# Optimization experiments

Hardware: AMD Instinct MI355X
Metric: run time of the kernel (lower is better)

Reference implementation:

```python
import jax, jax.numpy as jnp
import numpy as np

EMBED_DIM = 64
NUM_HEADS = 8
D_K = EMBED_DIM // NUM_HEADS  # 8
B, S = 8, 1024


def setup_inputs() -> dict:
    key = jax.random.key(0)
    ks = jax.random.split(key, 10)
    f32 = jnp.float32
    lim = 1.0 / np.sqrt(EMBED_DIM)
    def lin(k):
        kw, kb = jax.random.split(k)
        w = jax.random.uniform(kw, (EMBED_DIM, EMBED_DIM), f32, -lim, lim)
        b = jax.random.uniform(kb, (EMBED_DIM,), f32, -lim, lim)
        return w, b
    wq, bq = lin(ks[0])
    wk, bk = lin(ks[1])
    wv, bv = lin(ks[2])
    wo, bo = lin(ks[3])
    theta = jax.random.normal(ks[4], (EMBED_DIM,), f32)  # trainable RY angles, one per wire
    x = jax.random.normal(ks[5], (B, S, EMBED_DIM), f32)
    return {"x": x, "wq": wq, "bq": bq, "wk": wk, "bk": bk,
            "wv": wv, "bv": bv, "theta": theta, "wo": wo, "bo": bo}


def _quantum_map(t, theta):
    # Per-qubit circuit on |0>: RX(t_i) encode, RY(theta_i), <PauliZ_i>.
    # Product state => <Z_i> = cos(theta_i) * cos(t_i) exactly.
    return jnp.cos(theta) * jnp.cos(t.reshape(-1, EMBED_DIM))  # [N, E]


def reference(x, wq, bq, wk, bk, wv, bv, theta, wo, bo):
    # Linear QKV (torch nn.Linear: x @ W^T + b)
    q = x @ wq.T + bq
    k = x @ wk.T + bk
    v = x @ wv.T + bv
    # Quantum measurement map, flattened over batch*seq (as in the original)
    q_q = _quantum_map(q, theta)  # [N, E], N = B*S
    k_q = _quantum_map(k, theta)
    v_q = _quantum_map(v, theta)
    # Full flattened attention: [N, N] scores (original never reshapes back)
    scores = (q_q @ k_q.T) / jnp.sqrt(jnp.asarray(D_K, x.dtype))
    attn = jax.nn.softmax(scores, axis=-1)  # dropout is identity in eval
    out = attn @ v_q  # [N, E]
    return out @ wo.T + bo
```

## Files before the change

kernel.cpp:

```cpp
#include <hip/hip_runtime.h>
#include <hip/hip_bf16.h>

#define NQ 8192
#define DIM 64
#define SPLITS 16
#define QBLK 128
#define WQ 64
#define BN 64
#define KEYS_PER_SPLIT (NQ / SPLITS)
#define NTILES (KEYS_PER_SPLIT / BN)
#define GRID_FLASH ((NQ / QBLK) * SPLITS)
#define MERGEB 256
#define MROWS (NQ / MERGEB)
#define SC2 0.51012301920911057f
#define KSTR 72

typedef short s8v __attribute__((ext_vector_type(8)));
typedef short s4v __attribute__((ext_vector_type(4)));
typedef float f4v __attribute__((ext_vector_type(4)));
typedef int   i4v __attribute__((ext_vector_type(4)));
typedef int   i2v __attribute__((ext_vector_type(2)));

__device__ __forceinline__ float b2f(short s) {
  unsigned int u = ((unsigned int)(unsigned short)s) << 16;
  return __uint_as_float(u);
}
__device__ __forceinline__ short f2b(float f) {
  __hip_bfloat16 h = __float2bfloat16(f);
  return *reinterpret_cast<short*>(&h);
}
__device__ __forceinline__ int pack_bf16x2(float a, float b) {
  union { __hip_bfloat162 h; int i; } u;
  u.h = __float22bfloat162_rn(make_float2(a, b));
  return u.i;
}

#define QROWS 16
__global__ __launch_bounds__(256) void qkv_kernel(
    const float* __restrict__ x,
    const float* __restrict__ wq, const float* __restrict__ bq,
    const float* __restrict__ wk, const float* __restrict__ bk,
    const float* __restrict__ wv, const float* __restrict__ bv,
    const float* __restrict__ theta,
    short* __restrict__ qq, short* __restrict__ kvT) {
  __shared__ __align__(16) short wsh[3][DIM][KSTR];
  __shared__ __align__(16) short xsb[QROWS][DIM];
  int tid = threadIdx.x;
  for (int i = tid; i < 3 * DIM * 16; i += 256) {
    int m = i >> 10;
    int rem = i & 1023;
    int r = rem >> 4, c4 = (rem & 15) << 2;
    const float* src = (m == 0) ? wq : (m == 1) ? wk : wv;
    float4 w = *(const float4*)&src[r * DIM + c4];
    s4v p = {f2b(w.x), f2b(w.y), f2b(w.z), f2b(w.w)};
    *(s4v*)&wsh[m][r][c4] = p;
  }
  int rowbase = blockIdx.x * QROWS;
  for (int i = tid; i < QROWS * 16; i += 256) {
    int r = i >> 4, c4 = (i & 15) << 2;
    float4 v = *(const float4*)&x[(rowbase + r) * DIM + c4];
    s4v p = {f2b(v.x), f2b(v.y), f2b(v.z), f2b(v.w)};
    *(s4v*)&xsb[r][c4] = p;
  }
  __syncthreads();
  int e = tid & 63, rg = tid >> 6;
  float ct = __cosf(theta[e]);
  float bqv = bq[e], bkv = bk[e], bvv = bv[e];
  for (int r = rg; r < QROWS; r += 4) {
    float aq = bqv, ak = bkv, av = bvv;
#pragma unroll
    for (int c8 = 0; c8 < 8; ++c8) {
      s8v xv = *(const s8v*)&xsb[r][c8 * 8];
      s8v w0 = *(const s8v*)&wsh[0][e][c8 * 8];
      s8v w1 = *(const s8v*)&wsh[1][e][c8 * 8];
      s8v w2 = *(const s8v*)&wsh[2][e][c8 * 8];
#pragma unroll
      for (int j = 0; j < 8; ++j) {
        float xf = b2f(xv[j]);
        aq += xf * b2f(w0[j]);
        ak += xf * b2f(w1[j]);
        av += xf * b2f(w2[j]);
      }
    }
    int n = rowbase + r;
    qq[n * DIM + e] = f2b(ct * __cosf(aq));
    size_t tb = (size_t)(n >> 6) * 8192;
    kvT[tb + ((n & 63) >> 4) * 1024 + (e >> 5) * 512 +
        ((e & 31) >> 3) * 128 + (n & 15) * 8 + (e & 7)] = f2b(ct * __cosf(ak));
    kvT[tb + 4096 + ((n & 32) >> 5) * 2048 + (e >> 4) * 512 +
        ((n & 15) >> 2) * 128 + (e & 15) * 8 +
        ((n & 3) | ((n & 16) >> 2))] = f2b(ct * __cosf(av));
  }
}

#if __has_builtin(__builtin_amdgcn_global_load_lds)
#define DMA_CHUNK(srcp, dstp) \
  __builtin_amdgcn_global_load_lds( \
      (const __attribute__((address_space(1))) void*)(srcp), \
      (__attribute__((address_space(3))) void*)(dstp), 16, 0, 0)
#else
#define DMA_CHUNK(srcp, dstp) \
  { *(s8v*)((short*)(dstp) + (threadIdx.x & 63) * 8) = \
        *(const s8v*)((const short*)(srcp)); }
#endif

__global__ __launch_bounds__(128, 2) void flash_kernel(
    const short* __restrict__ qq, const short* __restrict__ kvT,
    short* __restrict__ pO, short* __restrict__ pL) {
  __shared__ __align__(16) short lds[2][8192];

  int tid = threadIdx.x;
  int wave = tid >> 6, lane = tid & 63;
  int l15 = lane & 15, quad = lane >> 4;
  int qblock = blockIdx.x >> 4, split = blockIdx.x & 15;
  int qbase = qblock * QBLK + wave * WQ;

  s8v qf[4][2];
#pragma unroll
  for (int qt = 0; qt < 4; ++qt) {
    const short* qr = qq + (qbase + qt * 16 + l15) * DIM + quad * 8;
    qf[qt][0] = *(const s8v*)qr;
    qf[qt][1] = *(const s8v*)(qr + 32);
  }

  f4v o[4][4];
  float ls[4] = {0.f, 0.f, 0.f, 0.f};
#pragma unroll
  for (int qt = 0; qt < 4; ++qt)
#pragma unroll
    for (int c = 0; c < 4; ++c) o[qt][c] = (f4v){0.f, 0.f, 0.f, 0.f};

  int gt0 = split * NTILES;

#define STAGE(T, BUF)                                                        \
  {                                                                          \
    const short* s_ = kvT + (size_t)(gt0 + (T)) * 8192 + wave * 4096 +       \
                      lane * 8;                                              \
    short* d_ = &lds[BUF][wave * 4096];                                      \
    _Pragma("unroll") for (int c2 = 0; c2 < 8; ++c2)                         \
        DMA_CHUNK(s_ + c2 * 512, d_ + c2 * 512);                             \
  }

  STAGE(0, 0)

  for (int t = 0; t < NTILES; ++t) {
    __syncthreads();
    if (t + 1 < NTILES) STAGE(t + 1, (t + 1) & 1)

    const short* kb = lds[t & 1];
    const short* vb = lds[t & 1] + 4096;

#pragma unroll
    for (int kp = 0; kp < 2; ++kp) {
      i4v pai[4];
#pragma unroll
      for (int h = 0; h < 2; ++h) {
        int kt = kp * 2 + h;
        s8v kf0 = *(const s8v*)&kb[(kt * 2) * 512 + lane * 8];
        s8v kf1 = *(const s8v*)&kb[(kt * 2 + 1) * 512 + lane * 8];
#pragma unroll
        for (int qt = 0; qt < 4; ++qt) {
          f4v acc = (f4v){0.f, 0.f, 0.f, 0.f};
          acc = __builtin_amdgcn_mfma_f32_16x16x32_bf16(kf0, qf[qt][0], acc, 0, 0, 0);
          acc = __builtin_amdgcn_mfma_f32_16x16x32_bf16(kf1, qf[qt][1], acc, 0, 0, 0);
          float p0 = exp2f(acc[0] * SC2), p1 = exp2f(acc[1] * SC2);
          float p2 = exp2f(acc[2] * SC2), p3 = exp2f(acc[3] * SC2);
          ls[qt] += (p0 + p1) + (p2 + p3);
          pai[qt][h * 2]     = pack_bf16x2(p0, p1);
          pai[qt][h * 2 + 1] = pack_bf16x2(p2, p3);
        }
      }
#pragma unroll
      for (int c = 0; c < 4; ++c) {
        s8v vf = *(const s8v*)&vb[(kp * 4 + c) * 512 + lane * 8];
#pragma unroll
        for (int qt = 0; qt < 4; ++qt)
          o[qt][c] = __builtin_amdgcn_mfma_f32_16x16x32_bf16(
              __builtin_bit_cast(s8v, pai[qt]), vf, o[qt][c], 0, 0, 0);
      }
    }
  }

#pragma unroll
  for (int qt = 0; qt < 4; ++qt) {
    float v = ls[qt];
    v += __shfl_xor(v, 16);
    v += __shfl_xor(v, 32);
    ls[qt] = v;
  }

  size_t pb = ((size_t)split * 64 + qblock) * 8192;
#pragma unroll
  for (int qt = 0; qt < 4; ++qt) {
#pragma unroll
    for (int c = 0; c < 4; ++c) {
      i2v pk = {pack_bf16x2(o[qt][c][0], o[qt][c][1]),
                pack_bf16x2(o[qt][c][2], o[qt][c][3])};
      *(i2v*)&pO[pb + (size_t)(((wave * 4 + qt) * 4 + c) * 256 + lane * 4)] = pk;
    }
    if (quad == 0) pL[split * NQ + qbase + qt * 16 + l15] = f2b(ls[qt]);
  }
}

__global__ __launch_bounds__(256) void merge_kernel(
    const short* __restrict__ pO, const short* __restrict__ pL,
    const float* __restrict__ wo, const float* __restrict__ bo,
    float* __restrict__ out) {
  __shared__ __align__(16) short wsh[DIM * KSTR];
  __shared__ __align__(16) float att[MROWS * DIM];
  int tid = threadIdx.x;
  int q0 = blockIdx.x * MROWS;
  for (int i = tid; i < DIM * 16; i += 256) {
    int r = i >> 4, c4 = (i & 15) << 2;
    float4 w = *(const float4*)&wo[r * DIM + c4];
    s4v p = {f2b(w.x), f2b(w.y), f2b(w.z), f2b(w.w)};
    *(s4v*)&wsh[r * KSTR + c4] = p;
  }
  int e = tid & 63, rg = tid >> 6;
  int c = e >> 4, l15e = e & 15;
  for (int rr = rg; rr < MROWS; rr += 4) {
    int q = q0 + rr;
    int qb = q >> 7, wv = (q >> 6) & 1, qt = (q >> 4) & 3;
    int qd = (q >> 2) & 3, r = q & 3;
    size_t base = (size_t)qb * 8192 +
                  (size_t)(((wv * 4 + qt) * 4 + c) * 256 + (qd * 16 + l15e) * 4 + r);
    float s = 0.f, l = 0.f;
#pragma unroll
    for (int sp = 0; sp < SPLITS; ++sp) {
      s += b2f(pO[(size_t)sp * 64 * 8192 + base]);
      l += b2f(pL[sp * NQ + q]);
    }
    att[rr * DIM + e] = s / l;
  }
  __syncthreads();
  for (int rr = rg; rr < MROWS; rr += 4) {
    float acc = bo[e];
#pragma unroll
    for (int c8 = 0; c8 < 8; ++c8) {
      s8v w = *(const s8v*)&wsh[e * KSTR + c8 * 8];
      const float* ar = &att[rr * DIM + c8 * 8];
      acc += ar[0] * b2f(w[0]) + ar[1] * b2f(w[1]) + ar[2] * b2f(w[2]) + ar[3] * b2f(w[3])
           + ar[4] * b2f(w[4]) + ar[5] * b2f(w[5]) + ar[6] * b2f(w[6]) + ar[7] * b2f(w[7]);
    }
    out[(size_t)(q0 + rr) * DIM + e] = acc;
  }
}

extern "C" void kernel_launch(void* const* d_in, const int* in_sizes, int n_in,
                              void* d_out, int out_size, void* d_ws, size_t ws_size,
                              hipStream_t stream) {
  const float* x  = (const float*)d_in[0];
  const float* wq = (const float*)d_in[1];
  const float* bq = (const float*)d_in[2];
  const float* wk = (const float*)d_in[3];
  const float* bk = (const float*)d_in[4];
  const float* wv = (const float*)d_in[5];
  const float* bv = (const float*)d_in[6];
  const float* th = (const float*)d_in[7];
  const float* wo = (const float*)d_in[8];
  const float* bo = (const float*)d_in[9];

  char* ws = (char*)d_ws;
  short* qq  = (short*)(ws);
  short* kvT = (short*)(ws + (1u << 20));
  short* pO  = (short*)(ws + (3u << 20));
  short* pL  = (short*)(ws + (19u << 20));

  hipLaunchKernelGGL(qkv_kernel, dim3(NQ / QROWS), dim3(256), 0, stream,
                     x, wq, bq, wk, bk, wv, bv, th, qq, kvT);
  hipLaunchKernelGGL(flash_kernel, dim3(GRID_FLASH), dim3(128), 0, stream,
                     qq, kvT, pO, pL);
  hipLaunchKernelGGL(merge_kernel, dim3(MERGEB), dim3(256), 0, stream,
                     pO, pL, wo, bo, (float*)d_out);
}
```

Baseline: 134.0 us.

## Fold softmax scale into Q, compute row sums via MFMA, re-layout partials for merge

Moves the exp2 scale factor into the Q projection, so the flash loop no longer multiplies every score before exp. It also switches to the hardware exp2 builtin and gets the softmax denominators from an extra MFMA against a ones vector, replacing the per-element scalar adds and shuffles. Partial outputs and sums are now stored row-major as [query][split][dim], so the merge kernel can do vectorized contiguous loads with a shuffle reduction instead of 16 strided scalar loads per element. The trade-offs are scattered 2-byte stores in the flash epilogue, and row sums that now come from bf16-rounded probabilities.

```diff
diff --git a/kernel.cpp b/kernel.cpp
--- a/kernel.cpp
+++ b/kernel.cpp
@@ -19,7 +19,6 @@
 typedef short s4v __attribute__((ext_vector_type(4)));
 typedef float f4v __attribute__((ext_vector_type(4)));
 typedef int   i4v __attribute__((ext_vector_type(4)));
-typedef int   i2v __attribute__((ext_vector_type(2)));
 
 __device__ __forceinline__ float b2f(short s) {
   unsigned int u = ((unsigned int)(unsigned short)s) << 16;
@@ -33,6 +32,13 @@
   union { __hip_bfloat162 h; int i; } u;
   u.h = __float22bfloat162_rn(make_float2(a, b));
   return u.i;
+}
+__device__ __forceinline__ float fast_exp2(float x) {
+#if __has_builtin(__builtin_amdgcn_exp2f)
+  return __builtin_amdgcn_exp2f(x);
+#else
+  return exp2f(x);
+#endif
 }
 
 #define QROWS 16
@@ -83,7 +89,7 @@
       }
     }
     int n = rowbase + r;
-    qq[n * DIM + e] = f2b(ct * __cosf(aq));
+    qq[n * DIM + e] = f2b(SC2 * ct * __cosf(aq));
     size_t tb = (size_t)(n >> 6) * 8192;
     kvT[tb + ((n & 63) >> 4) * 1024 + (e >> 5) * 512 +
         ((e & 31) >> 3) * 128 + (n & 15) * 8 + (e & 7)] = f2b(ct * __cosf(ak));
@@ -123,12 +129,16 @@
     qf[qt][1] = *(const s8v*)(qr + 32);
   }
 
-  f4v o[4][4];
-  float ls[4] = {0.f, 0.f, 0.f, 0.f};
-#pragma unroll
-  for (int qt = 0; qt < 4; ++qt)
+  const short ONE = (short)0x3F80;
+  const s8v ones = {ONE, ONE, ONE, ONE, ONE, ONE, ONE, ONE};
+
+  f4v o[4][4], ol[4];
+#pragma unroll
+  for (int qt = 0; qt < 4; ++qt) {
+    ol[qt] = (f4v){0.f, 0.f, 0.f, 0.f};
 #pragma unroll
     for (int c = 0; c < 4; ++c) o[qt][c] = (f4v){0.f, 0.f, 0.f, 0.f};
+  }
 
   int gt0 = split * NTILES;
 
@@ -163,13 +173,14 @@
           f4v acc = (f4v){0.f, 0.f, 0.f, 0.f};
           acc = __builtin_amdgcn_mfma_f32_16x16x32_bf16(kf0, qf[qt][0], acc, 0, 0, 0);
           acc = __builtin_amdgcn_mfma_f32_16x16x32_bf16(kf1, qf[qt][1], acc, 0, 0, 0);
-          float p0 = exp2f(acc[0] * SC2), p1 = exp2f(acc[1] * SC2);
-          float p2 = exp2f(acc[2] * SC2), p3 = exp2f(acc[3] * SC2);
-          ls[qt] += (p0 + p1) + (p2 + p3);
-          pai[qt][h * 2]     = pack_bf16x2(p0, p1);
-          pai[qt][h * 2 + 1] = pack_bf16x2(p2, p3);
+          pai[qt][h * 2]     = pack_bf16x2(fast_exp2(acc[0]), fast_exp2(acc[1]));
+          pai[qt][h * 2 + 1] = pack_bf16x2(fast_exp2(acc[2]), fast_exp2(acc[3]));
         }
       }
+#pragma unroll
+      for (int qt = 0; qt < 4; ++qt)
+        ol[qt] = __builtin_amdgcn_mfma_f32_16x16x32_bf16(
+            __builtin_bit_cast(s8v, pai[qt]), ones, ol[qt], 0, 0, 0);
 #pragma unroll
       for (int c = 0; c < 4; ++c) {
         s8v vf = *(const s8v*)&vb[(kp * 4 + c) * 512 + lane * 8];
@@ -183,22 +194,14 @@
 
 #pragma unroll
   for (int qt = 0; qt < 4; ++qt) {
-    float v = ls[qt];
-    v += __shfl_xor(v, 16);
-    v += __shfl_xor(v, 32);
-    ls[qt] = v;
-  }
-
-  size_t pb = ((size_t)split * 64 + qblock) * 8192;
-#pragma unroll
-  for (int qt = 0; qt < 4; ++qt) {
-#pragma unroll
-    for (int c = 0; c < 4; ++c) {
-      i2v pk = {pack_bf16x2(o[qt][c][0], o[qt][c][1]),
-                pack_bf16x2(o[qt][c][2], o[qt][c][3])};
-      *(i2v*)&pO[pb + (size_t)(((wave * 4 + qt) * 4 + c) * 256 + lane * 4)] = pk;
-    }
-    if (quad == 0) pL[split * NQ + qbase + qt * 16 + l15] = f2b(ls[qt]);
+#pragma unroll
+    for (int r = 0; r < 4; ++r) {
+      int q = qbase + qt * 16 + quad * 4 + r;
+      short* dst = pO + (size_t)q * (SPLITS * DIM) + split * DIM;
+#pragma unroll
+      for (int c = 0; c < 4; ++c) dst[c * 16 + l15] = f2b(o[qt][c][r]);
+      if (l15 == 0) pL[(size_t)q * SPLITS + split] = f2b(ol[qt][r]);
+    }
   }
 }
 
@@ -216,23 +219,41 @@
     s4v p = {f2b(w.x), f2b(w.y), f2b(w.z), f2b(w.w)};
     *(s4v*)&wsh[r * KSTR + c4] = p;
   }
+  int wave = tid >> 6, j = tid & 63;
+#pragma unroll
+  for (int i = 0; i < MROWS / 4; ++i) {
+    int rr = wave * (MROWS / 4) + i;
+    int q = q0 + rr;
+    const short* prow = pO + (size_t)q * (SPLITS * DIM);
+    s8v v0 = *(const s8v*)&prow[j * 8];
+    s8v v1 = *(const s8v*)&prow[512 + j * 8];
+    float a[8];
+#pragma unroll
+    for (int m = 0; m < 8; ++m) a[m] = b2f(v0[m]) + b2f(v1[m]);
+#pragma unroll
+    for (int st = 8; st < 64; st <<= 1)
+#pragma unroll
+      for (int m = 0; m < 8; ++m) a[m] += __shfl_xor(a[m], st);
+    const short* lrow = pL + (size_t)q * SPLITS;
+    s8v lv0 = *(const s8v*)&lrow[0];
+    s8v lv1 = *(const s8v*)&lrow[8];
+    float l = 0.f;
+#pragma unroll
+    for (int m = 0; m < 8; ++m) l += b2f(lv0[m]) + b2f(lv1[m]);
+#if __has_builtin(__builtin_amdgcn_rcpf)
+    float ri = __builtin_amdgcn_rcpf(l);
+#else
+    float ri = 1.f / l;
+#endif
+    if (j < 8) {
+      float4 f0 = {a[0] * ri, a[1] * ri, a[2] * ri, a[3] * ri};
+      float4 f1 = {a[4] * ri, a[5] * ri, a[6] * ri, a[7] * ri};
+      *(float4*)&att[rr * DIM + j * 8] = f0;
+      *(float4*)&att[rr * DIM + j * 8 + 4] = f1;
+    }
+  }
+  __syncthreads();
   int e = tid & 63, rg = tid >> 6;
-  int c = e >> 4, l15e = e & 15;
-  for (int rr = rg; rr < MROWS; rr += 4) {
-    int q = q0 + rr;
-    int qb = q >> 7, wv = (q >> 6) & 1, qt = (q >> 4) & 3;
-    int qd = (q >> 2) & 3, r = q & 3;
-    size_t base = (size_t)qb * 8192 +
-                  (size_t)(((wv * 4 + qt) * 4 + c) * 256 + (qd * 16 + l15e) * 4 + r);
-    float s = 0.f, l = 0.f;
-#pragma unroll
-    for (int sp = 0; sp < SPLITS; ++sp) {
-      s += b2f(pO[(size_t)sp * 64 * 8192 + base]);
-      l += b2f(pL[sp * NQ + q]);
-    }
-    att[rr * DIM + e] = s / l;
-  }
-  __syncthreads();
   for (int rr = rg; rr < MROWS; rr += 4) {
     float acc = bo[e];
 #pragma unroll
```

Result: faster. 121.6 us (median of 2 runs) (-9.2%).
